# Kernel optimization log

Measured on AMD Instinct MI355X. Metric: run time of the kernel, lower is better.

The kernel has to match this reference:

```python
import jax, jax.numpy as jnp
import numpy as np

N_NODES = 100000
N_FEAT = 128
HIDDEN = 64
OUT = 16
N_EDGES = 3200000
N_POS = 500000
N_NEG = 500000


def setup_inputs() -> dict:
    key = jax.random.key(0)
    ks = jax.random.split(key, 8)
    x = jax.random.normal(ks[0], (N_NODES, N_FEAT), dtype=jnp.float32)
    edge_index = jax.random.randint(ks[1], (2, N_EDGES), 0, N_NODES, dtype=jnp.int64)
    pos_edge_index = jax.random.randint(ks[2], (2, N_POS), 0, N_NODES, dtype=jnp.int64)
    neg_edge_index = jax.random.randint(ks[3], (2, N_NEG), 0, N_NODES, dtype=jnp.int64)
    W1 = jax.random.normal(ks[4], (N_FEAT, HIDDEN), dtype=jnp.float32) * (1.0 / np.sqrt(N_FEAT))
    b1 = jnp.zeros((HIDDEN,), dtype=jnp.float32)
    W2 = jax.random.normal(ks[5], (HIDDEN, OUT), dtype=jnp.float32) * (1.0 / np.sqrt(HIDDEN))
    b2 = jnp.zeros((OUT,), dtype=jnp.float32)
    return {"x": x, "edge_index": edge_index, "pos_edge_index": pos_edge_index,
            "neg_edge_index": neg_edge_index, "W1": W1, "b1": b1, "W2": W2, "b2": b2}


def gcn_conv(x, W, b, src, dst):
    """PyG GCNConv with add_self_loops=True: D^-1/2 (A+I) D^-1/2 X W + b."""
    n = x.shape[0]
    h = x @ W  # [N, out]
    # degree including self-loop (+1)
    deg = jax.ops.segment_sum(jnp.ones(dst.shape, dtype=h.dtype), dst, num_segments=n) + 1.0
    dis = jax.lax.rsqrt(deg)  # deg >= 1, never inf
    coef = dis[src] * dis[dst]  # [E]
    agg = jax.ops.segment_sum(h[src] * coef[:, None], dst, num_segments=n)
    # self-loop message: norm = dis[i]*dis[i]
    agg = agg + h * (dis * dis)[:, None]
    return agg + b


def reference(x, edge_index, pos_edge_index, neg_edge_index, W1, b1, W2, b2):
    src, dst = edge_index[0], edge_index[1]
    z = jax.nn.relu(gcn_conv(x, W1, b1, src, dst))
    z = gcn_conv(z, W2, b2, src, dst)  # [N, 16]
    ei = jnp.concatenate([pos_edge_index, neg_edge_index], axis=-1)  # [2, P+Q]
    logits = jnp.sum(z[ei[0]] * z[ei[1]], axis=-1)  # [P+Q]
    return logits
```

## Files before the change

kernel.cpp:

```cpp
#include <hip/hip_runtime.h>

#define F 128
#define H 64
#define O 16

#define BSHIFT 7
#define BSZ 128
#define NSUB 16
#define SUBCAP 384
#define ACHUNK 8192
#define XS 136

typedef _Float16 half8_t __attribute__((ext_vector_type(8)));
typedef _Float16 half4_t __attribute__((ext_vector_type(4)));
typedef float f32x4 __attribute__((ext_vector_type(4)));

#define MIX2(alo, ahi, dw)                                                              \
    do {                                                                                \
        asm("v_fma_mix_f32 %0, %1, 1.0, %0 op_sel_hi:[1,0,0]"                           \
            : "+v"(alo) : "v"(dw));                                                     \
        asm("v_fma_mix_f32 %0, %1, 1.0, %0 op_sel:[1,0,0] op_sel_hi:[1,0,0]"            \
            : "+v"(ahi) : "v"(dw));                                                     \
    } while (0)

#define MIXROW(r)                                                                       \
    do {                                                                                \
        MIX2(acc[0], acc[1], (r).x);                                                    \
        MIX2(acc[2], acc[3], (r).y);                                                    \
        MIX2(acc[4], acc[5], (r).z);                                                    \
        MIX2(acc[6], acc[7], (r).w);                                                    \
    } while (0)

__global__ void k_prep(const float* __restrict__ W1, _Float16* __restrict__ wt_hi,
                       _Float16* __restrict__ wt_lo, int* __restrict__ bcur, int NC) {
    int i = blockIdx.x * blockDim.x + threadIdx.x;
    if (i < NC) bcur[i] = i * SUBCAP;
    if (i < H * F) {
        int c = i >> 7, k = i & 127;
        float w = W1[k * H + c];
        _Float16 hi = (_Float16)w;
        wt_hi[i] = hi;
        wt_lo[i] = (_Float16)(w - (float)hi);
    }
}

__global__ __launch_bounds__(512) void k_bucketA(const int* __restrict__ src,
                                                 const int* __restrict__ dstv,
                                                 int* __restrict__ bcur,
                                                 int* __restrict__ bdata, int E) {
    __shared__ int hist[1024];
    for (int t = threadIdx.x; t < 1024; t += 512) hist[t] = 0;
    __syncthreads();
    int base = blockIdx.x * ACHUNK;
    int end = min(base + ACHUNK, E);
    int tid = threadIdx.x;
    int4 s4r[4], d4r[4];
    bool ok[4];
#pragma unroll
    for (int k = 0; k < 4; k++) {
        int i = base + tid * 4 + k * 2048;
        ok[k] = (i + 3 < end);
        if (ok[k]) {
            d4r[k] = *(const int4*)(dstv + i);
            s4r[k] = *(const int4*)(src + i);
            atomicAdd(&hist[d4r[k].x >> BSHIFT], 1);
            atomicAdd(&hist[d4r[k].y >> BSHIFT], 1);
            atomicAdd(&hist[d4r[k].z >> BSHIFT], 1);
            atomicAdd(&hist[d4r[k].w >> BSHIFT], 1);
        }
    }
    for (int i = base + ((end - base) & ~3) + tid; i < end; i += 512)
        atomicAdd(&hist[dstv[i] >> BSHIFT], 1);
    __syncthreads();
    int sub = blockIdx.x & (NSUB - 1);
    for (int b = tid; b < 1024; b += 512) {
        int c = hist[b];
        if (c > 0) hist[b] = atomicAdd(&bcur[b * NSUB + sub], c);
    }
    __syncthreads();
#pragma unroll
    for (int k = 0; k < 4; k++) {
        if (ok[k]) {
            int4 s4 = s4r[k];
            int4 d4 = d4r[k];
            int p0 = atomicAdd(&hist[d4.x >> BSHIFT], 1);
            bdata[p0] = (s4.x << BSHIFT) | (d4.x & (BSZ - 1));
            int p1 = atomicAdd(&hist[d4.y >> BSHIFT], 1);
            bdata[p1] = (s4.y << BSHIFT) | (d4.y & (BSZ - 1));
            int p2 = atomicAdd(&hist[d4.z >> BSHIFT], 1);
            bdata[p2] = (s4.z << BSHIFT) | (d4.z & (BSZ - 1));
            int p3 = atomicAdd(&hist[d4.w >> BSHIFT], 1);
            bdata[p3] = (s4.w << BSHIFT) | (d4.w & (BSZ - 1));
        }
    }
    for (int i = base + ((end - base) & ~3) + tid; i < end; i += 512) {
        int d = dstv[i];
        int pos = atomicAdd(&hist[d >> BSHIFT], 1);
        bdata[pos] = (src[i] << BSHIFT) | (d & (BSZ - 1));
    }
}

__global__ void k_bscan(const int* __restrict__ bcur, int* __restrict__ bstart, int NBK) {
    __shared__ int wsum[16];
    int tid = threadIdx.x;
    int lane = tid & 63, wv = tid >> 6;
    int tot = 0;
    if (tid < NBK) {
        for (int ss = 0; ss < NSUB; ss++)
            tot += bcur[tid * NSUB + ss] - (tid * NSUB + ss) * SUBCAP;
    }
    int val = tot;
#pragma unroll
    for (int off = 1; off < 64; off <<= 1) {
        int u = __shfl_up(val, off);
        if (lane >= off) val += u;
    }
    if (lane == 63) wsum[wv] = val;
    __syncthreads();
    int add = 0;
    for (int j = 0; j < wv; j++) add += wsum[j];
    bstart[tid] = val + add - tot;
}

__global__ __launch_bounds__(256) void k_bplace(const int* __restrict__ bdata,
                                                const int* __restrict__ bcur,
                                                const int* __restrict__ bstart,
                                                int* __restrict__ row_ptr,
                                                float* __restrict__ dis,
                                                int* __restrict__ col, int N) {
    __shared__ int h[BSZ];
    __shared__ int pref[BSZ];
    __shared__ int cur[BSZ];
    int b = blockIdx.x;
    int node0 = b << BSHIFT;
    int nloc = min(BSZ, N - node0);
    int tid = threadIdx.x;
    if (tid < BSZ) h[tid] = 0;
    __syncthreads();
    for (int s = 0; s < NSUB; s++) {
        int start = (b * NSUB + s) * SUBCAP;
        int end = bcur[b * NSUB + s];
        for (int p = start + tid; p < end; p += 256)
            atomicAdd(&h[bdata[p] & (BSZ - 1)], 1);
    }
    __syncthreads();
    int myDeg = 0;
    if (tid < BSZ) {
        myDeg = h[tid];
        pref[tid] = myDeg;
    }
    __syncthreads();
    for (int off = 1; off < BSZ; off <<= 1) {
        int v = (tid < BSZ && tid >= off) ? pref[tid - off] : 0;
        __syncthreads();
        if (tid < BSZ) pref[tid] += v;
        __syncthreads();
    }
    int base = bstart[b];
    if (tid < nloc) {
        int excl = base + pref[tid] - myDeg;
        cur[tid] = excl;
        row_ptr[node0 + tid] = excl;
        dis[node0 + tid] = rsqrtf((float)myDeg + 1.0f);
    }
    if (tid == 0) row_ptr[node0 + nloc] = base + pref[BSZ - 1];
    __syncthreads();
    for (int s = 0; s < NSUB; s++) {
        int start = (b * NSUB + s) * SUBCAP;
        int end = bcur[b * NSUB + s];
        for (int p = start + tid; p < end; p += 256) {
            int v = bdata[p];
            int pos = atomicAdd(&cur[v & (BSZ - 1)], 1);
            col[pos] = v >> BSHIFT;
        }
    }
}

__global__ __launch_bounds__(256) void k_gemm1(const float* __restrict__ x,
                                               const _Float16* __restrict__ wt_hi,
                                               const _Float16* __restrict__ wt_lo,
                                               const float* __restrict__ dis,
                                               _Float16* __restrict__ h1p, int N) {
    __shared__ _Float16 xh[64 * XS], xl[64 * XS], wh[64 * XS], wl[64 * XS];
    int tid = threadIdx.x;
    int row0 = blockIdx.x * 64;
#pragma unroll
    for (int i = 0; i < 8; i++) {
        int idx = i * 256 + tid;
        int r = idx >> 5;
        int c = (idx & 31) * 4;
        int rr = row0 + r; if (rr >= N) rr = N - 1;
        float4 v = *(const float4*)(x + (size_t)rr * F + c);
        half4_t h = {(_Float16)v.x, (_Float16)v.y, (_Float16)v.z, (_Float16)v.w};
        half4_t l = {(_Float16)(v.x - (float)h[0]), (_Float16)(v.y - (float)h[1]),
                     (_Float16)(v.z - (float)h[2]), (_Float16)(v.w - (float)h[3])};
        *(half4_t*)(xh + r * XS + c) = h;
        *(half4_t*)(xl + r * XS + c) = l;
    }
#pragma unroll
    for (int i = 0; i < 4; i++) {
        int idx = i * 256 + tid;
        int c = idx >> 4;
        int k8 = (idx & 15) * 8;
        *(half8_t*)(wh + c * XS + k8) = *(const half8_t*)(wt_hi + c * 128 + k8);
        *(half8_t*)(wl + c * XS + k8) = *(const half8_t*)(wt_lo + c * 128 + k8);
    }
    __syncthreads();
    int wv = tid >> 6, lane = tid & 63;
    int m = lane & 15, qd = lane >> 4;
    const _Float16* xhp = xh + (wv * 16 + m) * XS;
    const _Float16* xlp = xl + (wv * 16 + m) * XS;
    f32x4 acc[4] = {f32x4{0,0,0,0}, f32x4{0,0,0,0}, f32x4{0,0,0,0}, f32x4{0,0,0,0}};
#pragma unroll
    for (int kc = 0; kc < 4; kc++) {
        int ko = kc * 32 + qd * 8;
        half8_t ah = *(const half8_t*)(xhp + ko);
        half8_t al = *(const half8_t*)(xlp + ko);
#pragma unroll
        for (int nt = 0; nt < 4; nt++) {
            half8_t bh = *(const half8_t*)(wh + (nt * 16 + m) * XS + ko);
            half8_t bl = *(const half8_t*)(wl + (nt * 16 + m) * XS + ko);
            acc[nt] = __builtin_amdgcn_mfma_f32_16x16x32_f16(ah, bh, acc[nt], 0, 0, 0);
            acc[nt] = __builtin_amdgcn_mfma_f32_16x16x32_f16(ah, bl, acc[nt], 0, 0, 0);
            acc[nt] = __builtin_amdgcn_mfma_f32_16x16x32_f16(al, bh, acc[nt], 0, 0, 0);
        }
    }
#pragma unroll
    for (int reg = 0; reg < 4; reg++) {
        int row = row0 + wv * 16 + qd * 4 + reg;
        if (row < N) {
            float d = dis[row];
#pragma unroll
            for (int nt = 0; nt < 4; nt++) {
                h1p[(size_t)row * H + nt * 16 + m] = (_Float16)(acc[nt][reg] * d);
            }
        }
    }
}

__global__ __launch_bounds__(256) void k_gather1(const _Float16* __restrict__ h1p,
                                                 const float* __restrict__ dis,
                                                 const int* __restrict__ row_ptr,
                                                 const int* __restrict__ col,
                                                 const float* __restrict__ b1,
                                                 const float* __restrict__ W2,
                                                 _Float16* __restrict__ h2p, int N) {
    __shared__ float w2t[16 * 65];
    int tid = threadIdx.x;
    {
        int idx = tid * 4;
        float4 v = *(const float4*)(W2 + idx);
        const float* vp = (const float*)&v;
#pragma unroll
        for (int i = 0; i < 4; i++) {
            int e = idx + i;
            w2t[(e & 15) * 65 + (e >> 4)] = vp[i];
        }
    }
    __syncthreads();
    int lane = tid & 63;
    int h = lane >> 5;
    int g2 = (lane >> 3) & 3;
    int g = lane >> 3;
    int t = lane & 7;
    unsigned t16 = (unsigned)t * 16;
    const char* hb = (const char*)h1p;
    int hsign = 1 - 2 * h;
    float bb[8];
#pragma unroll
    for (int j = 0; j < 8; j++) bb[j] = b1[t * 8 + j];
    float w1v[8], w2v[8];
#pragma unroll
    for (int j = 0; j < 8; j++) {
        w1v[j] = w2t[g * 65 + t * 8 + j];
        w2v[j] = w2t[(g + 8) * 65 + t * 8 + j];
    }

    for (int node = blockIdx.x * 8 + (tid >> 6) * 2 + h; node < N; node += gridDim.x * 8) {
        float acc[8];
#pragma unroll
        for (int j = 0; j < 8; j++) acc[j] = 0.f;
        int e = row_ptr[node + 1];
        int p = row_ptr[node] + g2;
        for (; p + 12 < e; p += 16) {
            int s0 = col[p], s1 = col[p + 4], s2 = col[p + 8], s3 = col[p + 12];
            int4 r0 = *(const int4*)(hb + (((unsigned)s0 << 7) + t16));
            int4 r1 = *(const int4*)(hb + (((unsigned)s1 << 7) + t16));
            int4 r2 = *(const int4*)(hb + (((unsigned)s2 << 7) + t16));
            int4 r3 = *(const int4*)(hb + (((unsigned)s3 << 7) + t16));
            MIXROW(r0); MIXROW(r1); MIXROW(r2); MIXROW(r3);
        }
        for (; p + 4 < e; p += 8) {
            int s0 = col[p], s1 = col[p + 4];
            int4 r0 = *(const int4*)(hb + (((unsigned)s0 << 7) + t16));
            int4 r1 = *(const int4*)(hb + (((unsigned)s1 << 7) + t16));
            MIXROW(r0); MIXROW(r1);
        }
        if (p < e) {
            int s0 = col[p];
            int4 r0 = *(const int4*)(hb + (((unsigned)s0 << 7) + t16));
            MIXROW(r0);
        }
        if (g2 == 0) {
            int4 rs = *(const int4*)(hb + (((unsigned)node << 7) + t16));
            MIXROW(rs);
        }
#pragma unroll
        for (int off = 8; off < 32; off <<= 1) {
#pragma unroll
            for (int j = 0; j < 8; j++) acc[j] += __shfl_xor(acc[j], off);
        }
        float dn = dis[node];
        float o[8];
#pragma unroll
        for (int j = 0; j < 8; j++)
            o[j] = fmaxf(fmaf(acc[j], dn, bb[j]), 0.f);
        float oo[8];
#pragma unroll
        for (int j = 0; j < 8; j++) oo[j] = __shfl_xor(o[j], 32);
        float dno = __shfl_xor(dn, 32);
        float p1o = 0.f, p2o = 0.f, p1x = 0.f, p2x = 0.f;
#pragma unroll
        for (int j = 0; j < 8; j++) {
            p1o = fmaf(o[j], w1v[j], p1o);
            p2o = fmaf(o[j], w2v[j], p2o);
            p1x = fmaf(oo[j], w1v[j], p1x);
            p2x = fmaf(oo[j], w2v[j], p2x);
        }
#pragma unroll
        for (int off = 1; off < 8; off <<= 1) {
            p1o += __shfl_xor(p1o, off);
            p2o += __shfl_xor(p2o, off);
            p1x += __shfl_xor(p1x, off);
            p2x += __shfl_xor(p2x, off);
        }
        if (t == 0) {
            h2p[(size_t)node * O + g]     = (_Float16)(p1o * dn);
            h2p[(size_t)node * O + g + 8] = (_Float16)(p2o * dn);
            int nodeo = node + hsign;
            if (nodeo < N) {
                h2p[(size_t)nodeo * O + g]     = (_Float16)(p1x * dno);
                h2p[(size_t)nodeo * O + g + 8] = (_Float16)(p2x * dno);
            }
        }
    }
}

__global__ __launch_bounds__(256) void k_gather2(const _Float16* __restrict__ h2p,
                                                 const float* __restrict__ dis,
                                                 const int* __restrict__ row_ptr,
                                                 const int* __restrict__ col,
                                                 const float* __restrict__ b2,
                                                 float* __restrict__ z2, int N) {
    int tid = threadIdx.x;
    int lane = tid & 63;
    int g = lane >> 1;
    int t = lane & 1;
    unsigned t16 = (unsigned)t * 16;
    const char* hb = (const char*)h2p;
    float bb[8];
#pragma unroll
    for (int j = 0; j < 8; j++) bb[j] = b2[t * 8 + j];

    for (int node = blockIdx.x * 4 + (tid >> 6); node < N; node += gridDim.x * 4) {
        float acc[8];
#pragma unroll
        for (int j = 0; j < 8; j++) acc[j] = 0.f;
        int e = row_ptr[node + 1];
        for (int p = row_ptr[node] + g; p < e; p += 32) {
            int s = col[p];
            int4 r = *(const int4*)(hb + (((unsigned)s << 5) + t16));
            MIXROW(r);
        }
        if (g == 0) {
            int4 rs = *(const int4*)(hb + (((unsigned)node << 5) + t16));
            MIXROW(rs);
        }
#pragma unroll
        for (int off = 2; off < 64; off <<= 1) {
#pragma unroll
            for (int j = 0; j < 8; j++) acc[j] += __shfl_xor(acc[j], off);
        }
        if (g == 0) {
            float dn = dis[node];
            float o[8];
#pragma unroll
            for (int j = 0; j < 8; j++)
                o[j] = fmaf(acc[j], dn, bb[j]);
            float4* zp = (float4*)(z2 + (size_t)node * O + t * 8);
            zp[0] = float4{o[0], o[1], o[2], o[3]};
            zp[1] = float4{o[4], o[5], o[6], o[7]};
        }
    }
}

__global__ __launch_bounds__(256) void k_logits(const float* __restrict__ z2,
                                                const int* __restrict__ pos,
                                                const int* __restrict__ neg,
                                                float* __restrict__ out, int P, int Q) {
    int tid = blockIdx.x * 256 + threadIdx.x;
    int i = tid >> 2;
    if (i >= P + Q) return;
    int k = tid & 3;
    unsigned k16 = (unsigned)k * 16;
    const char* zb = (const char*)z2;
    int a, b;
    if (i < P) { a = pos[i]; b = pos[P + i]; }
    else       { int t = i - P; a = neg[t]; b = neg[Q + t]; }
    float4 va = *(const float4*)(zb + (((unsigned)a << 6) + k16));
    float4 vb = *(const float4*)(zb + (((unsigned)b << 6) + k16));
    float r = va.x * vb.x + va.y * vb.y + va.z * vb.z + va.w * vb.w;
    r += __shfl_xor(r, 1);
    r += __shfl_xor(r, 2);
    if (k == 0) out[i] = r;
}

extern "C" void kernel_launch(void* const* d_in, const int* in_sizes, int n_in,
                              void* d_out, int out_size, void* d_ws, size_t ws_size,
                              hipStream_t stream) {
    const float* x   = (const float*)d_in[0];
    const int*   ei  = (const int*)d_in[1];
    const int*   pos = (const int*)d_in[2];
    const int*   neg = (const int*)d_in[3];
    const float* W1  = (const float*)d_in[4];
    const float* b1  = (const float*)d_in[5];
    const float* W2  = (const float*)d_in[6];
    const float* b2  = (const float*)d_in[7];
    float* out = (float*)d_out;

    int N = in_sizes[0] / F;
    int E = in_sizes[1] / 2;
    int P = in_sizes[2] / 2;
    int Q = in_sizes[3] / 2;
    const int* src  = ei;
    const int* dstv = ei + E;

    int Npad = ((N + 255) / 256) * 256;
    int Epad = (E + 63) & ~63;
    int NBK = (N + BSZ - 1) / BSZ;
    int NC  = NBK * NSUB;

    char* w = (char*)d_ws;
    float*    dis     = (float*)w;    w += (size_t)Npad * 4;
    int*      row_ptr = (int*)w;      w += (size_t)(Npad + 256) * 4;
    int*      bcur    = (int*)w;      w += 16384 * 4;
    int*      bstart  = (int*)w;      w += 1024 * 4;
    int*      col     = (int*)w;      w += (size_t)Epad * 4;
    _Float16* h1p     = (_Float16*)w;
    int*      bdata   = (int*)w;
    size_t h1b = (size_t)N * H * 2, bdb = (size_t)NC * SUBCAP * 4;
    w += (h1b > bdb ? h1b : bdb);
    _Float16* h2p     = (_Float16*)w; w += (size_t)N * O * 2;
    float*    z2      = (float*)w;    w += (size_t)N * O * 4;
    _Float16* wt_hi   = (_Float16*)w; w += (size_t)H * F * 2;
    _Float16* wt_lo   = (_Float16*)w;

    int prepN = (NC > H * F) ? NC : H * F;

    k_prep<<<(prepN + 255) / 256, 256, 0, stream>>>(W1, wt_hi, wt_lo, bcur, NC);
    k_bucketA<<<(E + ACHUNK - 1) / ACHUNK, 512, 0, stream>>>(src, dstv, bcur, bdata, E);
    k_bscan<<<1, 1024, 0, stream>>>(bcur, bstart, NBK);
    k_bplace<<<NBK, 256, 0, stream>>>(bdata, bcur, bstart, row_ptr, dis, col, N);

    k_gemm1<<<(N + 63) / 64, 256, 0, stream>>>(x, wt_hi, wt_lo, dis, h1p, N);
    k_gather1<<<2048, 256, 0, stream>>>(h1p, dis, row_ptr, col, b1, W2, h2p, N);
    k_gather2<<<(N + 3) / 4, 256, 0, stream>>>(h2p, dis, row_ptr, col, b2, z2, N);
    k_logits<<<((P + Q) * 4 + 255) / 256, 256, 0, stream>>>(z2, pos, neg, out, P, Q);
}
```

Baseline: 306.5 us.

## Fold bucket scan into placement kernel and deepen gather1 unroll with row_ptr prefetch

Removes the single-block k_bscan launch. Each k_bplace block now computes its own bucket start by reducing the counts of all earlier sub-buckets, which saves one launch and a serialization point but adds redundant work that grows with block index. In k_gather1, the next node's row_ptr values are prefetched across loop iterations, and an 8-way unrolled edge loop is added to put more neighbor loads in flight.

```diff
diff --git a/kernel.cpp b/kernel.cpp
--- a/kernel.cpp
+++ b/kernel.cpp
@@ -100,43 +100,31 @@
     }
 }
 
-__global__ void k_bscan(const int* __restrict__ bcur, int* __restrict__ bstart, int NBK) {
-    __shared__ int wsum[16];
-    int tid = threadIdx.x;
-    int lane = tid & 63, wv = tid >> 6;
-    int tot = 0;
-    if (tid < NBK) {
-        for (int ss = 0; ss < NSUB; ss++)
-            tot += bcur[tid * NSUB + ss] - (tid * NSUB + ss) * SUBCAP;
-    }
-    int val = tot;
-#pragma unroll
-    for (int off = 1; off < 64; off <<= 1) {
-        int u = __shfl_up(val, off);
-        if (lane >= off) val += u;
-    }
-    if (lane == 63) wsum[wv] = val;
-    __syncthreads();
-    int add = 0;
-    for (int j = 0; j < wv; j++) add += wsum[j];
-    bstart[tid] = val + add - tot;
-}
-
 __global__ __launch_bounds__(256) void k_bplace(const int* __restrict__ bdata,
                                                 const int* __restrict__ bcur,
-                                                const int* __restrict__ bstart,
                                                 int* __restrict__ row_ptr,
                                                 float* __restrict__ dis,
                                                 int* __restrict__ col, int N) {
     __shared__ int h[BSZ];
     __shared__ int pref[BSZ];
     __shared__ int cur[BSZ];
+    __shared__ int red[256];
     int b = blockIdx.x;
     int node0 = b << BSHIFT;
     int nloc = min(BSZ, N - node0);
     int tid = threadIdx.x;
+    int partial = 0;
+    int limit = b * NSUB;
+    for (int i = tid; i < limit; i += 256)
+        partial += bcur[i] - i * SUBCAP;
+    red[tid] = partial;
     if (tid < BSZ) h[tid] = 0;
     __syncthreads();
+    for (int off = 128; off > 0; off >>= 1) {
+        if (tid < off) red[tid] += red[tid + off];
+        __syncthreads();
+    }
+    int base = red[0];
     for (int s = 0; s < NSUB; s++) {
         int start = (b * NSUB + s) * SUBCAP;
         int end = bcur[b * NSUB + s];
@@ -156,7 +144,6 @@
         if (tid < BSZ) pref[tid] += v;
         __syncthreads();
     }
-    int base = bstart[b];
     if (tid < nloc) {
         int excl = base + pref[tid] - myDeg;
         cur[tid] = excl;
@@ -276,12 +263,33 @@
         w2v[j] = w2t[(g + 8) * 65 + t * 8 + j];
     }
 
-    for (int node = blockIdx.x * 8 + (tid >> 6) * 2 + h; node < N; node += gridDim.x * 8) {
+    int stride = gridDim.x * 8;
+    int node = blockIdx.x * 8 + (tid >> 6) * 2 + h;
+    int rpA = 0, rpB = 0;
+    if (node < N) { rpA = row_ptr[node]; rpB = row_ptr[node + 1]; }
+    while (node < N) {
+        int nnode = node + stride;
+        int nA = 0, nB = 0;
+        if (nnode < N) { nA = row_ptr[nnode]; nB = row_ptr[nnode + 1]; }
         float acc[8];
 #pragma unroll
         for (int j = 0; j < 8; j++) acc[j] = 0.f;
-        int e = row_ptr[node + 1];
-        int p = row_ptr[node] + g2;
+        int e = rpB;
+        int p = rpA + g2;
+        for (; p + 28 < e; p += 32) {
+            int s0 = col[p],      s1 = col[p + 4],  s2 = col[p + 8],  s3 = col[p + 12];
+            int s4 = col[p + 16], s5 = col[p + 20], s6 = col[p + 24], s7 = col[p + 28];
+            int4 r0 = *(const int4*)(hb + (((unsigned)s0 << 7) + t16));
+            int4 r1 = *(const int4*)(hb + (((unsigned)s1 << 7) + t16));
+            int4 r2 = *(const int4*)(hb + (((unsigned)s2 << 7) + t16));
+            int4 r3 = *(const int4*)(hb + (((unsigned)s3 << 7) + t16));
+            int4 r4 = *(const int4*)(hb + (((unsigned)s4 << 7) + t16));
+            int4 r5 = *(const int4*)(hb + (((unsigned)s5 << 7) + t16));
+            int4 r6 = *(const int4*)(hb + (((unsigned)s6 << 7) + t16));
+            int4 r7 = *(const int4*)(hb + (((unsigned)s7 << 7) + t16));
+            MIXROW(r0); MIXROW(r1); MIXROW(r2); MIXROW(r3);
+            MIXROW(r4); MIXROW(r5); MIXROW(r6); MIXROW(r7);
+        }
         for (; p + 12 < e; p += 16) {
             int s0 = col[p], s1 = col[p + 4], s2 = col[p + 8], s3 = col[p + 12];
             int4 r0 = *(const int4*)(hb + (((unsigned)s0 << 7) + t16));
@@ -343,6 +351,7 @@
                 h2p[(size_t)nodeo * O + g + 8] = (_Float16)(p2x * dno);
             }
         }
+        node = nnode; rpA = nA; rpB = nB;
     }
 }
 
@@ -444,7 +453,6 @@
     float*    dis     = (float*)w;    w += (size_t)Npad * 4;
     int*      row_ptr = (int*)w;      w += (size_t)(Npad + 256) * 4;
     int*      bcur    = (int*)w;      w += 16384 * 4;
-    int*      bstart  = (int*)w;      w += 1024 * 4;
     int*      col     = (int*)w;      w += (size_t)Epad * 4;
     _Float16* h1p     = (_Float16*)w;
     int*      bdata   = (int*)w;
@@ -459,8 +467,7 @@
 
     k_prep<<<(prepN + 255) / 256, 256, 0, stream>>>(W1, wt_hi, wt_lo, bcur, NC);
     k_bucketA<<<(E + ACHUNK - 1) / ACHUNK, 512, 0, stream>>>(src, dstv, bcur, bdata, E);
-    k_bscan<<<1, 1024, 0, stream>>>(bcur, bstart, NBK);
-    k_bplace<<<NBK, 256, 0, stream>>>(bdata, bcur, bstart, row_ptr, dis, col, N);
+    k_bplace<<<NBK, 256, 0, stream>>>(bdata, bcur, row_ptr, dis, col, N);
 
     k_gemm1<<<(N + 63) / 64, 256, 0, stream>>>(x, wt_hi, wt_lo, dis, h1p, N);
     k_gather1<<<2048, 256, 0, stream>>>(h1p, dis, row_ptr, col, b1, W2, h2p, N);
```

After: 307.2 us. No clear change (+0.2%).
